# Optimization experiments

Hardware: AMD Instinct MI355X
Metric: run time of the kernel (lower is better)

Reference implementation:

```python
import jax, jax.numpy as jnp
import numpy as np

B, S, D, DM, H, DH, DF, L, T = 4096, 64, 256, 512, 4, 64, 512, 6, 20


def mish(x):
    return x * jnp.tanh(jax.nn.softplus(x))


def layernorm(x, eps=1e-5):
    mu = jnp.mean(x, axis=-1, keepdims=True)
    var = jnp.var(x, axis=-1, keepdims=True)
    return (x - mu) * jax.lax.rsqrt(var + eps)


def setup_inputs() -> dict:
    key = jax.random.key(0)
    ks = iter(jax.random.split(key, 32))
    w = lambda *shape: jax.random.normal(next(ks), shape, dtype=jnp.float32) * 0.02
    inp = {
        'x_t': jax.random.normal(next(ks), (B, S, D), dtype=jnp.float32),
        't': jax.random.randint(next(ks), (B,), 0, T + 1),
        'backbone_latent': jax.random.normal(next(ks), (B, S, DM), dtype=jnp.float32),
        # timestep embedding
        'emb': w(T + 1, D),
        'te_w1': w(D, 4 * D), 'te_b1': jnp.zeros((4 * D,), jnp.float32),
        'te_w2': w(4 * D, D), 'te_b2': jnp.zeros((D,), jnp.float32),
        # cond projection
        'cp_w1': w(DM, D), 'cp_b1': jnp.zeros((D,), jnp.float32),
        'cp_w2': w(D, D), 'cp_b2': jnp.zeros((D,), jnp.float32),
        # stacked per-layer DiT block params [L, ...]
        'adaln_w': w(L, D, 6 * D), 'adaln_b': jnp.zeros((L, 6 * D), jnp.float32),
        'qkv_w': w(L, D, 3 * D), 'qkv_b': jnp.zeros((L, 3 * D), jnp.float32),
        'op_w': w(L, D, D), 'op_b': jnp.zeros((L, D), jnp.float32),
        'ffn_w1': w(L, D, DF), 'ffn_b1': jnp.zeros((L, DF), jnp.float32),
        'ffn_w2': w(L, DF, D), 'ffn_b2': jnp.zeros((L, D), jnp.float32),
        # final adaLN + projection (random here for nontrivial test, zero-init in original)
        'fa_w': w(D, 2 * D), 'fa_b': jnp.zeros((2 * D,), jnp.float32),
        'fp_w': w(D, D), 'fp_b': jnp.zeros((D,), jnp.float32),
    }
    return inp


def _forward(x_t, t, backbone_latent, emb, te_w1, te_b1, te_w2, te_b2,
             cp_w1, cp_b1, cp_w2, cp_b2, adaln_w, adaln_b, qkv_w, qkv_b,
             op_w, op_b, ffn_w1, ffn_b1, ffn_w2, ffn_b2, fa_w, fa_b, fp_w, fp_b):
    # conditioning vector c: [B, D]
    te = emb[t]                                   # [B, D]
    te = mish(te @ te_w1 + te_b1) @ te_w2 + te_b2
    cond = jnp.mean(backbone_latent, axis=1)      # [B, DM]
    cond = mish(cond @ cp_w1 + cp_b1) @ cp_w2 + cp_b2
    c = te + cond
    mc = mish(c)

    x = x_t
    for l in range(L):
        mod = (mc @ adaln_w[l] + adaln_b[l])[:, None, :]   # [B, 1, 6D]
        sh1, sc1, g1, sh2, sc2, g2 = jnp.split(mod, 6, axis=-1)
        # attention sub-block
        h = layernorm(x) * (1.0 + sc1) + sh1
        qkv = (h @ qkv_w[l] + qkv_b[l]).reshape(B, S, 3, H, DH)
        q = qkv[:, :, 0].transpose(0, 2, 1, 3)   # [B, H, S, DH]
        k = qkv[:, :, 1].transpose(0, 2, 1, 3)
        v = qkv[:, :, 2].transpose(0, 2, 1, 3)
        attn = jax.nn.softmax(jnp.einsum('bhsd,bhtd->bhst', q, k) * DH ** -0.5, axis=-1)
        h = jnp.einsum('bhst,bhtd->bhsd', attn, v).transpose(0, 2, 1, 3).reshape(B, S, D)
        h = h @ op_w[l] + op_b[l]
        x = x + g1 * h
        # FFN sub-block
        h = layernorm(x) * (1.0 + sc2) + sh2
        h = mish(h @ ffn_w1[l] + ffn_b1[l]) @ ffn_w2[l] + ffn_b2[l]
        x = x + g2 * h

    mod = (mc @ fa_w + fa_b)[:, None, :]
    shift, scale = jnp.split(mod, 2, axis=-1)
    x = layernorm(x) * (1.0 + scale) + shift
    return x @ fp_w + fp_b


def reference(x_t, t, backbone_latent, emb, te_w1, te_b1, te_w2, te_b2,
              cp_w1, cp_b1, cp_w2, cp_b2, adaln_w, adaln_b, qkv_w, qkv_b,
              op_w, op_b, ffn_w1, ffn_b1, ffn_w2, ffn_b2, fa_w, fa_b, fp_w, fp_b):
    return _forward(x_t, t, backbone_latent, emb, te_w1, te_b1, te_w2, te_b2,
                    cp_w1, cp_b1, cp_w2, cp_b2, adaln_w, adaln_b, qkv_w, qkv_b,
                    op_w, op_b, ffn_w1, ffn_b1, ffn_w2, ffn_b2, fa_w, fa_b, fp_w, fp_b)
```

## Files before the change

### kernel.cpp

```cpp
#include <hip/hip_runtime.h>

typedef unsigned short u16;
typedef float f32x4 __attribute__((ext_vector_type(4)));
typedef __bf16 bf16x8 __attribute__((ext_vector_type(8)));

__device__ __forceinline__ u16 f2b(float f) {
  unsigned u = __builtin_bit_cast(unsigned, f);
  u += 0x7FFF + ((u >> 16) & 1);
  return (u16)(u >> 16);
}

__device__ __forceinline__ float b2f(u16 v) {
  unsigned u = (unsigned)v << 16;
  return __builtin_bit_cast(float, u);
}

__device__ __forceinline__ f32x4 ld_bf4(const u16* p) {
  ushort4 v = *(const ushort4*)p;
  f32x4 r;
  r[0] = b2f(v.x); r[1] = b2f(v.y); r[2] = b2f(v.z); r[3] = b2f(v.w);
  return r;
}

__device__ __forceinline__ float mishf(float x) {
  float e = __expf(fminf(x, 20.f));
  float n = e * (e + 2.f);
  return x * __fdividef(n, n + 2.f);
}

__device__ __forceinline__ void gl_lds16(const void* g, void* l) {
  __builtin_amdgcn_global_load_lds((__attribute__((address_space(1))) void*)g,
                                   (__attribute__((address_space(3))) void*)l, 16, 0, 0);
}

__device__ __forceinline__ bf16x8 ldb8(const u16* p) {
  return __builtin_bit_cast(bf16x8, *(const uint4*)p);
}

__global__ __launch_bounds__(256)
void transpose_w(const float* __restrict__ in, u16* __restrict__ out, int K, int N) {
  __shared__ float tl[64][65];
  const long zoff = (long)blockIdx.z * K * N;
  in += zoff; out += zoff;
  const int n0 = blockIdx.x * 64, k0 = blockIdx.y * 64;
  const int c = threadIdx.x & 63, r0 = threadIdx.x >> 6;
#pragma unroll
  for (int i = 0; i < 16; ++i) {
    int r = i * 4 + r0;
    tl[r][c] = in[(long)(k0 + r) * N + n0 + c];
  }
  __syncthreads();
#pragma unroll
  for (int i = 0; i < 16; ++i) {
    int r = i * 4 + r0;
    out[(long)(n0 + r) * K + k0 + c] = f2b(tl[c][r]);
  }
}

__global__ __launch_bounds__(1024)
void te_table_kernel(const float* __restrict__ emb, const float* __restrict__ w1,
                     const float* __restrict__ b1, const float* __restrict__ w2,
                     const float* __restrict__ b2, float* __restrict__ table) {
  __shared__ float te[256];
  __shared__ float h1[1024];
  __shared__ float red[1024];
  const int tt = blockIdx.x, tid = threadIdx.x;
  if (tid < 256) te[tid] = emb[tt * 256 + tid];
  __syncthreads();
  float a = b1[tid];
#pragma unroll 8
  for (int k = 0; k < 256; ++k) a += te[k] * w1[k * 1024 + tid];
  h1[tid] = mishf(a);
  __syncthreads();
  const int j = tid & 255, kq = tid >> 8;
  float a2 = 0.f;
#pragma unroll 8
  for (int k = kq * 256; k < kq * 256 + 256; ++k) a2 += h1[k] * w2[k * 256 + j];
  red[tid] = a2;
  __syncthreads();
  if (tid < 256)
    table[tt * 256 + tid] = b2[tid] + red[tid] + red[tid + 256] + red[tid + 512] + red[tid + 768];
}

__global__ __launch_bounds__(256)
void cond_mean_kernel(const float* __restrict__ bb, u16* __restrict__ cond) {
  const int b = blockIdx.x, tid = threadIdx.x;
  const float* p = bb + (long)b * 64 * 512;
  for (int d = tid; d < 512; d += 256) {
    float s = 0.f;
#pragma unroll
    for (int t = 0; t < 64; ++t) s += p[t * 512 + d];
    cond[b * 512 + d] = f2b(s * (1.f / 64.f));
  }
}

__global__ __launch_bounds__(256)
void ln_mod(const float* __restrict__ x, const u16* __restrict__ modb,
            int mstride, int shoff, int scoff, u16* __restrict__ out) {
  const int lane = threadIdx.x & 63;
  const long row = (long)blockIdx.x * 4 + (threadIdx.x >> 6);
  const float4 xv = *(const float4*)(x + row * 256 + lane * 4);
  float s1 = xv.x + xv.y + xv.z + xv.w;
  float s2 = xv.x * xv.x + xv.y * xv.y + xv.z * xv.z + xv.w * xv.w;
#pragma unroll
  for (int m = 1; m < 64; m <<= 1) { s1 += __shfl_xor(s1, m); s2 += __shfl_xor(s2, m); }
  const float mean = s1 * (1.f / 256.f);
  float var = s2 * (1.f / 256.f) - mean * mean;
  const float rstd = rsqrtf(fmaxf(var, 0.f) + 1e-5f);
  const long b = row >> 6;
  const f32x4 sc = ld_bf4(modb + b * mstride + scoff + lane * 4);
  const f32x4 sh = ld_bf4(modb + b * mstride + shoff + lane * 4);
  ushort4 o;
  o.x = f2b((xv.x - mean) * rstd * (1.f + sc[0]) + sh[0]);
  o.y = f2b((xv.y - mean) * rstd * (1.f + sc[1]) + sh[1]);
  o.z = f2b((xv.z - mean) * rstd * (1.f + sc[2]) + sh[2]);
  o.w = f2b((xv.w - mean) * rstd * (1.f + sc[3]) + sh[3]);
  *(ushort4*)(out + row * 256 + lane * 4) = o;
}

template <int EPI>
__global__ __launch_bounds__(256)
void gemm_bt(const u16* __restrict__ A, const u16* __restrict__ Bt,
             const float* __restrict__ bias, void* __restrict__ outp,
             const int* __restrict__ tvec, const float* __restrict__ tetab,
             int M, int N, int K) {
  __shared__ __align__(16) u16 As[2][128 * 64];
  __shared__ __align__(16) u16 Bs[2][128 * 64];
  const int tid = threadIdx.x;
  const int lane = tid & 63;
  const int wave = tid >> 6;
  const int wr = (wave >> 1) << 6;
  const int wc = (wave & 1) << 6;
  const long tm = (long)blockIdx.y * 128;
  const long tn = (long)blockIdx.x * 128;
  const u16* Ag = A + tm * K;
  const u16* Bg = Bt + tn * K;
  f32x4 acc[4][4] = {};
  const int kcb = lane >> 4;
  const int swz = lane & 7;
  const int NT = K >> 6;

  auto stage = [&](int t, int buf) {
    const int k0 = t << 6;
#pragma unroll
    for (int i = 0; i < 4; ++i) {
      int c = tid + (i << 8);
      int r = c >> 3;
      int sch = (c & 7) ^ (r & 7);
      gl_lds16(Ag + (long)r * K + k0 + (sch << 3), &As[buf][c << 3]);
    }
#pragma unroll
    for (int i = 0; i < 4; ++i) {
      int c = tid + (i << 8);
      int r = c >> 3;
      int sch = (c & 7) ^ (r & 7);
      gl_lds16(Bg + (long)r * K + k0 + (sch << 3), &Bs[buf][c << 3]);
    }
  };

  stage(0, 0);
  __syncthreads();
  int cur = 0;
  for (int t = 0; t < NT; ++t) {
    if (t + 1 < NT) stage(t + 1, cur ^ 1);
#pragma unroll
    for (int kt = 0; kt < 2; ++kt) {
      const int ko = ((kt * 4 + kcb) ^ swz) << 3;
      bf16x8 av[4], bv[4];
#pragma unroll
      for (int mt = 0; mt < 4; ++mt)
        av[mt] = ldb8(&As[cur][(wr + mt * 16 + (lane & 15)) * 64 + ko]);
#pragma unroll
      for (int nt = 0; nt < 4; ++nt)
        bv[nt] = ldb8(&Bs[cur][(wc + nt * 16 + (lane & 15)) * 64 + ko]);
#pragma unroll
      for (int mt = 0; mt < 4; ++mt)
#pragma unroll
        for (int nt = 0; nt < 4; ++nt)
          acc[mt][nt] = __builtin_amdgcn_mfma_f32_16x16x32_bf16(bv[nt], av[mt], acc[mt][nt], 0, 0, 0);
    }
    __syncthreads();
    cur ^= 1;
  }
  const int rl = lane & 15;
  const int c4 = (lane >> 4) << 2;
  f32x4 b4[4];
#pragma unroll
  for (int nt = 0; nt < 4; ++nt)
    b4[nt] = *(const f32x4*)(bias + (int)tn + wc + nt * 16 + c4);
#pragma unroll
  for (int mt = 0; mt < 4; ++mt) {
    const unsigned row = (unsigned)(tm + wr + mt * 16 + rl);
    const unsigned rb = row * (unsigned)N;
#pragma unroll
    for (int nt = 0; nt < 4; ++nt) {
      const unsigned col = (unsigned)tn + wc + nt * 16 + c4;
      f32x4 v = acc[mt][nt] + b4[nt];
      if constexpr (EPI == 0) {
        ushort4 o;
        o.x = f2b(v[0]); o.y = f2b(v[1]); o.z = f2b(v[2]); o.w = f2b(v[3]);
        *(ushort4*)((u16*)outp + rb + col) = o;
      } else if constexpr (EPI == 1) {
        ushort4 o;
        o.x = f2b(mishf(v[0])); o.y = f2b(mishf(v[1]));
        o.z = f2b(mishf(v[2])); o.w = f2b(mishf(v[3]));
        *(ushort4*)((u16*)outp + rb + col) = o;
      } else if constexpr (EPI == 3) {
        *(f32x4*)((float*)outp + rb + col) = v;
      } else {
        const f32x4 te = *(const f32x4*)(tetab + tvec[row] * 256 + col);
        ushort4 o;
        o.x = f2b(mishf(v[0] + te[0])); o.y = f2b(mishf(v[1] + te[1]));
        o.z = f2b(mishf(v[2] + te[2])); o.w = f2b(mishf(v[3] + te[3]));
        *(ushort4*)((u16*)outp + rb + col) = o;
      }
    }
  }
}

template <int K, bool XF32>
__global__ __launch_bounds__(256)
void gemm_ln(const u16* __restrict__ A, const u16* __restrict__ Bt,
             const float* __restrict__ bias, const void* __restrict__ xin,
             const u16* __restrict__ gptr, int gstride,
             const u16* __restrict__ lnsh, const u16* __restrict__ lnsc, int lnstride,
             u16* __restrict__ xout, u16* __restrict__ hout) {
  __shared__ __align__(16) u16 As[2][64 * 64];
  __shared__ __align__(16) u16 Bs[2][256 * 64];
  const int tid = threadIdx.x, lane = tid & 63, wave = tid >> 6;
  const int wc = wave << 6;
  const long tm = (long)blockIdx.x * 64;
  const u16* Ag = A + tm * K;
  const int rl = lane & 15;
  const int c4 = (lane >> 4) << 2;
  const int swz = lane & 7;
  const int NT = K >> 6;

  auto stage = [&](int t, int buf) {
    const int k0 = t << 6;
#pragma unroll
    for (int i = 0; i < 2; ++i) {
      int c = tid + (i << 8);
      int r = c >> 3;
      int sch = (c & 7) ^ (r & 7);
      gl_lds16(Ag + (long)r * K + k0 + (sch << 3), &As[buf][c << 3]);
    }
#pragma unroll
    for (int i = 0; i < 8; ++i) {
      int c = tid + (i << 8);
      int r = c >> 3;
      int sch = (c & 7) ^ (r & 7);
      gl_lds16(Bt + (long)r * K + k0 + (sch << 3), &Bs[buf][c << 3]);
    }
  };

  stage(0, 0);
  __syncthreads();

  f32x4 acc[4][4] = {};
  int cur = 0;
  for (int t = 0; t < NT; ++t) {
    if (t + 1 < NT) stage(t + 1, cur ^ 1);
#pragma unroll
    for (int kt = 0; kt < 2; ++kt) {
      const int ko = ((kt * 4 + (lane >> 4)) ^ swz) << 3;
      bf16x8 av[4], bv[4];
#pragma unroll
      for (int mt = 0; mt < 4; ++mt)
        av[mt] = ldb8(&As[cur][(mt * 16 + rl) * 64 + ko]);
#pragma unroll
      for (int nt = 0; nt < 4; ++nt)
        bv[nt] = ldb8(&Bs[cur][(wc + nt * 16 + rl) * 64 + ko]);
#pragma unroll
      for (int mt = 0; mt < 4; ++mt)
#pragma unroll
        for (int nt = 0; nt < 4; ++nt)
          acc[mt][nt] = __builtin_amdgcn_mfma_f32_16x16x32_bf16(bv[nt], av[mt], acc[mt][nt], 0, 0, 0);
    }
    __syncthreads();
    cur ^= 1;
  }

  const long b = blockIdx.x;
  float s1[4] = {}, s2[4] = {};
#pragma unroll
  for (int nt = 0; nt < 4; ++nt) {
    const int col = wc + nt * 16 + c4;
    const f32x4 b4 = *(const f32x4*)(bias + col);
    const f32x4 g4 = ld_bf4(gptr + b * gstride + col);
#pragma unroll
    for (int mt = 0; mt < 4; ++mt) {
      const long row = tm + mt * 16 + rl;
      f32x4 x;
      if constexpr (XF32) x = *(const f32x4*)((const float*)xin + row * 256 + col);
      else x = ld_bf4((const u16*)xin + row * 256 + col);
      f32x4 xn = x + g4 * (acc[mt][nt] + b4);
      acc[mt][nt] = xn;
      s1[mt] += xn[0] + xn[1] + xn[2] + xn[3];
      s2[mt] += xn[0] * xn[0] + xn[1] * xn[1] + xn[2] * xn[2] + xn[3] * xn[3];
    }
  }
#pragma unroll
  for (int mt = 0; mt < 4; ++mt) {
    s1[mt] += __shfl_xor(s1[mt], 16); s1[mt] += __shfl_xor(s1[mt], 32);
    s2[mt] += __shfl_xor(s2[mt], 16); s2[mt] += __shfl_xor(s2[mt], 32);
  }
  float* st = (float*)&As[0][0];
  if (lane < 16) {
#pragma unroll
    for (int mt = 0; mt < 4; ++mt) {
      st[wave * 128 + mt * 16 + lane] = s1[mt];
      st[wave * 128 + 64 + mt * 16 + lane] = s2[mt];
    }
  }
  __syncthreads();
  float mean[4], rstd[4];
#pragma unroll
  for (int mt = 0; mt < 4; ++mt) {
    float a = 0.f, q = 0.f;
#pragma unroll
    for (int w2 = 0; w2 < 4; ++w2) {
      a += st[w2 * 128 + mt * 16 + rl];
      q += st[w2 * 128 + 64 + mt * 16 + rl];
    }
    mean[mt] = a * (1.f / 256.f);
    float var = q * (1.f / 256.f) - mean[mt] * mean[mt];
    rstd[mt] = rsqrtf(fmaxf(var, 0.f) + 1e-5f);
  }
#pragma unroll
  for (int nt = 0; nt < 4; ++nt) {
    const int col = wc + nt * 16 + c4;
    const f32x4 sc4 = ld_bf4(lnsc + b * lnstride + col);
    const f32x4 sh4 = ld_bf4(lnsh + b * lnstride + col);
#pragma unroll
    for (int mt = 0; mt < 4; ++mt) {
      const long row = tm + mt * 16 + rl;
      ushort4 xo;
      xo.x = f2b(acc[mt][nt][0]); xo.y = f2b(acc[mt][nt][1]);
      xo.z = f2b(acc[mt][nt][2]); xo.w = f2b(acc[mt][nt][3]);
      *(ushort4*)(xout + row * 256 + col) = xo;
      f32x4 h = (acc[mt][nt] - mean[mt]) * rstd[mt] * (1.f + sc4) + sh4;
      ushort4 o;
      o.x = f2b(h[0]); o.y = f2b(h[1]); o.z = f2b(h[2]); o.w = f2b(h[3]);
      *(ushort4*)(hout + row * 256 + col) = o;
    }
  }
}

__global__ __launch_bounds__(512)
void ffn_fused(const u16* __restrict__ xln, const u16* __restrict__ W1t,
               const float* __restrict__ b1, const u16* __restrict__ W2t,
               const float* __restrict__ b2, const u16* __restrict__ xres,
               const u16* __restrict__ gptr, int gstride,
               const u16* __restrict__ lnsh, const u16* __restrict__ lnsc, int lnstride,
               u16* __restrict__ xout, u16* __restrict__ hout) {
  __shared__ __align__(16) u16 Ax[64 * 256];
  __shared__ __align__(16) u16 Ws[2][256 * 64];
  __shared__ __align__(16) u16 H1[64 * 512];
  const int tid = threadIdx.x, lane = tid & 63, wave = tid >> 6;
  const long b0 = (long)blockIdx.x * 2;
  const int rl = lane & 15;
  const int c4 = (lane >> 4) << 2;
  const int kq = lane >> 4;

  auto stageAx = [&](long b) {
    const u16* src = xln + b * (64 * 256);
#pragma unroll
    for (int i = 0; i < 4; ++i) {
      int c = tid + (i << 9);
      int r = c >> 5, cc = c & 31;
      int sch = (cc & ~7) | ((cc & 7) ^ (r & 7));
      gl_lds16(src + r * 256 + (sch << 3), &Ax[c << 3]);
    }
  };
  auto stageW = [&](const u16* Wsrc, int Kw, int R0, int k0, int buf) {
#pragma unroll
    for (int i = 0; i < 4; ++i) {
      int c = tid + (i << 9);
      int r = c >> 3;
      int sch = (c & 7) ^ (r & 7);
      gl_lds16(Wsrc + (long)(R0 + r) * Kw + k0 + (sch << 3), &Ws[buf][c << 3]);
    }
  };

  stageAx(b0);
  stageW(W1t, 256, 0, 0, 0);
  __syncthreads();
  int cur = 0;

  for (int e = 0; e < 2; ++e) {
    const long b = b0 + e;
    for (int nh = 0; nh < 2; ++nh) {
      f32x4 acc[4][2] = {};
      for (int t = 0; t < 4; ++t) {
        int s = nh * 4 + t;
        if (s < 7) stageW(W1t, 256, ((s + 1) >> 2) * 256, ((s + 1) & 3) * 64, cur ^ 1);
        else stageW(W2t, 512, 0, 0, cur ^ 1);
#pragma unroll
        for (int kt = 0; kt < 2; ++kt) {
          bf16x8 av[4], bv[2];
#pragma unroll
          for (int mt = 0; mt < 4; ++mt) {
            int r = mt * 16 + rl;
            int kc = t * 8 + kt * 4 + kq;
            int slot = (kc & ~7) | ((kc & 7) ^ (r & 7));
            av[mt] = ldb8(&Ax[r * 256 + (slot << 3)]);
          }
#pragma unroll
          for (int nf = 0; nf < 2; ++nf) {
            int wr_ = wave * 32 + nf * 16 + rl;
            int slot = (kt * 4 + kq) ^ (wr_ & 7);
            bv[nf] = ldb8(&Ws[cur][wr_ * 64 + (slot << 3)]);
          }
#pragma unroll
          for (int mt = 0; mt < 4; ++mt)
#pragma unroll
            for (int nf = 0; nf < 2; ++nf)
              acc[mt][nf] = __builtin_amdgcn_mfma_f32_16x16x32_bf16(bv[nf], av[mt], acc[mt][nf], 0, 0, 0);
        }
        __syncthreads();
        cur ^= 1;
      }
#pragma unroll
      for (int nf = 0; nf < 2; ++nf) {
        const int col = nh * 256 + wave * 32 + nf * 16 + c4;
        const f32x4 bb = *(const f32x4*)(b1 + col);
        const int c8 = col >> 3;
        const int sub = (col & 7) << 1;
#pragma unroll
        for (int mt = 0; mt < 4; ++mt) {
          const int r = mt * 16 + rl;
          f32x4 v = acc[mt][nf] + bb;
          ushort4 o;
          o.x = f2b(mishf(v[0])); o.y = f2b(mishf(v[1]));
          o.z = f2b(mishf(v[2])); o.w = f2b(mishf(v[3]));
          int slot = (c8 & ~7) | ((c8 & 7) ^ (r & 7));
          *(ushort4*)((char*)H1 + r * 1024 + (slot << 4) + sub) = o;
        }
      }
    }
    __syncthreads();

    f32x4 acc[4][2] = {};
    for (int t = 0; t < 8; ++t) {
      if (t < 7) stageW(W2t, 512, 0, (t + 1) * 64, cur ^ 1);
      else if (e == 0) stageW(W1t, 256, 0, 0, cur ^ 1);
      if (t == 0 && e == 0) stageAx(b0 + 1);
#pragma unroll
      for (int kt = 0; kt < 2; ++kt) {
        bf16x8 av[4], bv[2];
#pragma unroll
        for (int mt = 0; mt < 4; ++mt) {
          int r = mt * 16 + rl;
          int kc = t * 8 + kt * 4 + kq;
          int slot = (kc & ~7) | ((kc & 7) ^ (r & 7));
          av[mt] = ldb8((const u16*)((const char*)H1 + r * 1024 + (slot << 4)));
        }
#pragma unroll
        for (int nf = 0; nf < 2; ++nf) {
          int wr_ = wave * 32 + nf * 16 + rl;
          int slot = (kt * 4 + kq) ^ (wr_ & 7);
          bv[nf] = ldb8(&Ws[cur][wr_ * 64 + (slot << 3)]);
        }
#pragma unroll
        for (int mt = 0; mt < 4; ++mt)
#pragma unroll
          for (int nf = 0; nf < 2; ++nf)
            acc[mt][nf] = __builtin_amdgcn_mfma_f32_16x16x32_bf16(bv[nf], av[mt], acc[mt][nf], 0, 0, 0);
      }
      __syncthreads();
      cur ^= 1;
    }
    float s1[4] = {}, s2[4] = {};
#pragma unroll
    for (int nf = 0; nf < 2; ++nf) {
      const int col = wave * 32 + nf * 16 + c4;
      const f32x4 bb = *(const f32x4*)(b2 + col);
      const f32x4 g4 = ld_bf4(gptr + b * gstride + col);
#pragma unroll
      for (int mt = 0; mt < 4; ++mt) {
        const long row = b * 64 + mt * 16 + rl;
        f32x4 x = ld_bf4(xres + row * 256 + col);
        f32x4 xn = x + g4 * (acc[mt][nf] + bb);
        acc[mt][nf] = xn;
        s1[mt] += xn[0] + xn[1] + xn[2] + xn[3];
        s2[mt] += xn[0] * xn[0] + xn[1] * xn[1] + xn[2] * xn[2] + xn[3] * xn[3];
      }
    }
#pragma unroll
    for (int mt = 0; mt < 4; ++mt) {
      s1[mt] += __shfl_xor(s1[mt], 16); s1[mt] += __shfl_xor(s1[mt], 32);
      s2[mt] += __shfl_xor(s2[mt], 16); s2[mt] += __shfl_xor(s2[mt], 32);
    }
    float* st = (float*)&H1[0];
    if (lane < 16) {
#pragma unroll
      for (int mt = 0; mt < 4; ++mt) {
        st[wave * 128 + mt * 16 + lane] = s1[mt];
        st[wave * 128 + 64 + mt * 16 + lane] = s2[mt];
      }
    }
    __syncthreads();
    float mean[4], rstd[4];
#pragma unroll
    for (int mt = 0; mt < 4; ++mt) {
      float a = 0.f, q = 0.f;
#pragma unroll
      for (int w2 = 0; w2 < 8; ++w2) {
        a += st[w2 * 128 + mt * 16 + rl];
        q += st[w2 * 128 + 64 + mt * 16 + rl];
      }
      mean[mt] = a * (1.f / 256.f);
      float var = q * (1.f / 256.f) - mean[mt] * mean[mt];
      rstd[mt] = rsqrtf(fmaxf(var, 0.f) + 1e-5f);
    }
#pragma unroll
    for (int nf = 0; nf < 2; ++nf) {
      const int col = wave * 32 + nf * 16 + c4;
      const f32x4 sc4 = ld_bf4(lnsc + b * lnstride + col);
      const f32x4 sh4 = ld_bf4(lnsh + b * lnstride + col);
#pragma unroll
      for (int mt = 0; mt < 4; ++mt) {
        const long row = b * 64 + mt * 16 + rl;
        ushort4 xo;
        xo.x = f2b(acc[mt][nf][0]); xo.y = f2b(acc[mt][nf][1]);
        xo.z = f2b(acc[mt][nf][2]); xo.w = f2b(acc[mt][nf][3]);
        *(ushort4*)(xout + row * 256 + col) = xo;
        f32x4 h = (acc[mt][nf] - mean[mt]) * rstd[mt] * (1.f + sc4) + sh4;
        ushort4 o;
        o.x = f2b(h[0]); o.y = f2b(h[1]); o.z = f2b(h[2]); o.w = f2b(h[3]);
        *(ushort4*)(hout + row * 256 + col) = o;
      }
    }
    __syncthreads();
  }
}

__global__ __launch_bounds__(128)
void attn_kernel(const u16* __restrict__ qkv, u16* __restrict__ out) {
  __shared__ __align__(16) u16 vt_s[2][64 * 72];
  __shared__ __align__(16) u16 p_s[2][64 * 72];
  const int lane = threadIdx.x & 63;
  const int wave = threadIdx.x >> 6;
  const long b = blockIdx.x >> 1;
  const int h = ((blockIdx.x & 1) << 1) | wave;
  u16* vt = vt_s[wave];
  u16* pl = p_s[wave];
  const u16* base = qkv + b * (64 * 768);
#pragma unroll
  for (int it = 0; it < 8; ++it) {
    int chunk = it * 64 + lane;
    int t = chunk >> 3, dhb = (chunk & 7) << 3;
    union { uint4 u; u16 s[8]; } uv;
    uv.u = *(const uint4*)(base + t * 768 + 512 + h * 64 + dhb);
#pragma unroll
    for (int j = 0; j < 8; ++j) vt[(dhb + j) * 72 + t] = uv.s[j];
  }
  const u16* qb = base + h * 64;
  const u16* kb = base + 256 + h * 64;
  f32x4 sacc[4][4] = {};
#pragma unroll
  for (int kt = 0; kt < 2; ++kt) {
    bf16x8 qa[4], kv[4];
#pragma unroll
    for (int mt = 0; mt < 4; ++mt)
      qa[mt] = ldb8(qb + ((lane & 15) + mt * 16) * 768 + kt * 32 + ((lane >> 4) << 3));
#pragma unroll
    for (int nt = 0; nt < 4; ++nt)
      kv[nt] = ldb8(kb + ((lane & 15) + nt * 16) * 768 + kt * 32 + ((lane >> 4) << 3));
#pragma unroll
    for (int mt = 0; mt < 4; ++mt)
#pragma unroll
      for (int nt = 0; nt < 4; ++nt)
        sacc[mt][nt] = __builtin_amdgcn_mfma_f32_16x16x32_bf16(qa[mt], kv[nt], sacc[mt][nt], 0, 0, 0);
  }
  const float scale = 0.125f;
#pragma unroll
  for (int mt = 0; mt < 4; ++mt) {
#pragma unroll
    for (int r = 0; r < 4; ++r) {
      float mx = fmaxf(fmaxf(sacc[mt][0][r], sacc[mt][1][r]), fmaxf(sacc[mt][2][r], sacc[mt][3][r]));
#pragma unroll
      for (int m = 1; m <= 8; m <<= 1) mx = fmaxf(mx, __shfl_xor(mx, m));
      float p[4];
      float sum = 0.f;
#pragma unroll
      for (int nt = 0; nt < 4; ++nt) { p[nt] = __expf((sacc[mt][nt][r] - mx) * scale); sum += p[nt]; }
#pragma unroll
      for (int m = 1; m <= 8; m <<= 1) sum += __shfl_xor(sum, m);
      const float rinv = 1.f / sum;
      const int s = mt * 16 + ((lane >> 4) << 2) + r;
#pragma unroll
      for (int nt = 0; nt < 4; ++nt) pl[s * 72 + nt * 16 + (lane & 15)] = f2b(p[nt] * rinv);
    }
  }
  __syncthreads();
  f32x4 oacc[4][4] = {};
#pragma unroll
  for (int kt = 0; kt < 2; ++kt) {
    bf16x8 pa[4], vv[4];
#pragma unroll
    for (int mt = 0; mt < 4; ++mt)
      pa[mt] = ldb8(pl + ((lane & 15) + mt * 16) * 72 + kt * 32 + ((lane >> 4) << 3));
#pragma unroll
    for (int nt = 0; nt < 4; ++nt)
      vv[nt] = ldb8(vt + ((lane & 15) + nt * 16) * 72 + kt * 32 + ((lane >> 4) << 3));
#pragma unroll
    for (int mt = 0; mt < 4; ++mt)
#pragma unroll
      for (int nt = 0; nt < 4; ++nt)
        oacc[mt][nt] = __builtin_amdgcn_mfma_f32_16x16x32_bf16(vv[nt], pa[mt], oacc[mt][nt], 0, 0, 0);
  }
  u16* ob = out + b * (64 * 256) + h * 64;
#pragma unroll
  for (int mt = 0; mt < 4; ++mt)
#pragma unroll
    for (int nt = 0; nt < 4; ++nt) {
      const int s = mt * 16 + (lane & 15);
      const int d4 = nt * 16 + ((lane >> 4) << 2);
      ushort4 o;
      o.x = f2b(oacc[mt][nt][0]); o.y = f2b(oacc[mt][nt][1]);
      o.z = f2b(oacc[mt][nt][2]); o.w = f2b(oacc[mt][nt][3]);
      *(ushort4*)(ob + s * 256 + d4) = o;
    }
}

extern "C" void kernel_launch(void* const* d_in, const int* in_sizes, int n_in,
                              void* d_out, int out_size, void* d_ws, size_t ws_size,
                              hipStream_t stream) {
  (void)in_sizes; (void)n_in; (void)out_size; (void)ws_size;
  const int B = 4096, L = 6;
  const long BSr = (long)B * 64;

  const float* x_t = (const float*)d_in[0];
  const int* tvec = (const int*)d_in[1];
  const float* backbone = (const float*)d_in[2];
  const float* emb = (const float*)d_in[3];
  const float* te_w1 = (const float*)d_in[4];
  const float* te_b1 = (const float*)d_in[5];
  const float* te_w2 = (const float*)d_in[6];
  const float* te_b2 = (const float*)d_in[7];
  const float* cp_w1 = (const float*)d_in[8];
  const float* cp_b1 = (const float*)d_in[9];
  const float* cp_w2 = (const float*)d_in[10];
  const float* cp_b2 = (const float*)d_in[11];
  const float* adaln_w = (const float*)d_in[12];
  const float* adaln_b = (const float*)d_in[13];
  const float* qkv_w = (const float*)d_in[14];
  const float* qkv_b = (const float*)d_in[15];
  const float* op_w = (const float*)d_in[16];
  const float* op_b = (const float*)d_in[17];
  const float* ffn_w1 = (const float*)d_in[18];
  const float* ffn_b1 = (const float*)d_in[19];
  const float* ffn_w2 = (const float*)d_in[20];
  const float* ffn_b2 = (const float*)d_in[21];
  const float* fa_w = (const float*)d_in[22];
  const float* fa_b = (const float*)d_in[23];
  const float* fp_w = (const float*)d_in[24];
  const float* fp_b = (const float*)d_in[25];

  char* w = (char*)d_ws;
  auto alloc = [&](size_t bytes) { char* p = w; w += (bytes + 255) & ~(size_t)255; return p; };
  u16* WT_cp1 = (u16*)alloc(256L * 512 * 2);
  u16* WT_cp2 = (u16*)alloc(256L * 256 * 2);
  u16* WT_adaln = (u16*)alloc(6L * 1536 * 256 * 2);
  u16* WT_qkv = (u16*)alloc(6L * 768 * 256 * 2);
  u16* WT_op = (u16*)alloc(6L * 256 * 256 * 2);
  u16* WT_f1 = (u16*)alloc(6L * 512 * 256 * 2);
  u16* WT_f2 = (u16*)alloc(6L * 256 * 512 * 2);
  u16* WT_fa = (u16*)alloc(512L * 256 * 2);
  u16* WT_fp = (u16*)alloc(256L * 256 * 2);
  float* te_tab = (float*)alloc(21L * 256 * 4);
  u16* cond = (u16*)alloc(4096L * 512 * 2);
  u16* c1 = (u16*)alloc(4096L * 256 * 2);
  u16* mc = (u16*)alloc(4096L * 256 * 2);
  u16* modb6 = (u16*)alloc(4096L * 9216 * 2);
  u16* famod = (u16*)alloc(4096L * 512 * 2);
  u16* hbuf = (u16*)alloc(BSr * 256 * 2);
  u16* qkvbuf = (u16*)alloc(BSr * 768 * 2);
  u16* xbuf = (u16*)d_out;

  transpose_w<<<dim3(4, 8, 1), 256, 0, stream>>>(cp_w1, WT_cp1, 512, 256);
  transpose_w<<<dim3(4, 4, 1), 256, 0, stream>>>(cp_w2, WT_cp2, 256, 256);
  transpose_w<<<dim3(24, 4, 6), 256, 0, stream>>>(adaln_w, WT_adaln, 256, 1536);
  transpose_w<<<dim3(12, 4, 6), 256, 0, stream>>>(qkv_w, WT_qkv, 256, 768);
  transpose_w<<<dim3(4, 4, 6), 256, 0, stream>>>(op_w, WT_op, 256, 256);
  transpose_w<<<dim3(8, 4, 6), 256, 0, stream>>>(ffn_w1, WT_f1, 256, 512);
  transpose_w<<<dim3(4, 8, 6), 256, 0, stream>>>(ffn_w2, WT_f2, 512, 256);
  transpose_w<<<dim3(8, 4, 1), 256, 0, stream>>>(fa_w, WT_fa, 256, 512);
  transpose_w<<<dim3(4, 4, 1), 256, 0, stream>>>(fp_w, WT_fp, 256, 256);

  te_table_kernel<<<21, 1024, 0, stream>>>(emb, te_w1, te_b1, te_w2, te_b2, te_tab);
  cond_mean_kernel<<<4096, 256, 0, stream>>>(backbone, cond);

  gemm_bt<1><<<dim3(2, 32), 256, 0, stream>>>(cond, WT_cp1, cp_b1, c1, nullptr, nullptr, 4096, 256, 512);
  gemm_bt<4><<<dim3(2, 32), 256, 0, stream>>>(c1, WT_cp2, cp_b2, mc, tvec, te_tab, 4096, 256, 256);
  gemm_bt<0><<<dim3(4, 32), 256, 0, stream>>>(mc, WT_fa, fa_b, famod, nullptr, nullptr, 4096, 512, 256);
  gemm_bt<0><<<dim3(72, 32), 256, 0, stream>>>(mc, WT_adaln, adaln_b, modb6, nullptr, nullptr, 4096, 9216, 256);

  ln_mod<<<BSr / 4, 256, 0, stream>>>(x_t, modb6, 9216, 0, 256, hbuf);

  for (int l = 0; l < L; ++l) {
    const u16* mb = modb6 + (long)l * 1536;
    gemm_bt<0><<<dim3(6, BSr / 128), 256, 0, stream>>>(hbuf, WT_qkv + (long)l * 768 * 256, qkv_b + l * 768,
                                                       qkvbuf, nullptr, nullptr, (int)BSr, 768, 256);
    attn_kernel<<<B * 2, 128, 0, stream>>>(qkvbuf, hbuf);
    if (l == 0)
      gemm_ln<256, true><<<BSr / 64, 256, 0, stream>>>(hbuf, WT_op, op_b, x_t, mb + 512, 9216,
                                                       mb + 768, mb + 1024, 9216, xbuf, hbuf);
    else
      gemm_ln<256, false><<<BSr / 64, 256, 0, stream>>>(hbuf, WT_op + (long)l * 256 * 256, op_b + l * 256,
                                                        xbuf, mb + 512, 9216, mb + 768, mb + 1024, 9216, xbuf, hbuf);
    const u16* nsh = (l < 5) ? (mb + 1536) : famod;
    const u16* nsc = (l < 5) ? (mb + 1536 + 256) : (famod + 256);
    const int nstride = (l < 5) ? 9216 : 512;
    ffn_fused<<<BSr / 128, 512, 0, stream>>>(hbuf, WT_f1 + (long)l * 512 * 256, ffn_b1 + l * 512,
                                             WT_f2 + (long)l * 256 * 512, ffn_b2 + l * 256,
                                             xbuf, mb + 1280, 9216, nsh, nsc, nstride, xbuf, hbuf);
  }
  gemm_bt<3><<<dim3(2, BSr / 128), 256, 0, stream>>>(hbuf, WT_fp, fp_b, d_out, nullptr, nullptr, (int)BSr, 256, 256);
}
```

Baseline: 6.250 ms.

## Merge final adaLN GEMM into adaLN GEMM; process two batches per gemm_ln block

```diff
diff --git a/kernel.cpp b/kernel.cpp
--- a/kernel.cpp
+++ b/kernel.cpp
@@ -55,6 +55,14 @@
     int r = i * 4 + r0;
     out[(long)(n0 + r) * K + k0 + c] = f2b(tl[c][r]);
   }
+}
+
+__global__ __launch_bounds__(256)
+void concat_bias(const float* __restrict__ a, const float* __restrict__ b,
+                 float* __restrict__ out) {
+  int i = blockIdx.x * 256 + threadIdx.x;
+  if (i < 9216) out[i] = a[i];
+  else if (i < 9728) out[i] = b[i - 9216];
 }
 
 __global__ __launch_bounds__(1024)
@@ -229,14 +237,14 @@
   __shared__ __align__(16) u16 Bs[2][256 * 64];
   const int tid = threadIdx.x, lane = tid & 63, wave = tid >> 6;
   const int wc = wave << 6;
-  const long tm = (long)blockIdx.x * 64;
-  const u16* Ag = A + tm * K;
+  const long b0 = (long)blockIdx.x * 2;
   const int rl = lane & 15;
   const int c4 = (lane >> 4) << 2;
   const int swz = lane & 7;
   const int NT = K >> 6;
 
-  auto stage = [&](int t, int buf) {
+  auto stageA = [&](long b, int t, int buf) {
+    const u16* Ag = A + b * 64 * K;
     const int k0 = t << 6;
 #pragma unroll
     for (int i = 0; i < 2; ++i) {
@@ -245,6 +253,9 @@
       int sch = (c & 7) ^ (r & 7);
       gl_lds16(Ag + (long)r * K + k0 + (sch << 3), &As[buf][c << 3]);
     }
+  };
+  auto stageB = [&](int t, int buf) {
+    const int k0 = t << 6;
 #pragma unroll
     for (int i = 0; i < 8; ++i) {
       int c = tid + (i << 8);
@@ -254,96 +265,102 @@
     }
   };
 
-  stage(0, 0);
+  stageA(b0, 0, 0);
+  stageB(0, 0);
   __syncthreads();
-
-  f32x4 acc[4][4] = {};
   int cur = 0;
-  for (int t = 0; t < NT; ++t) {
-    if (t + 1 < NT) stage(t + 1, cur ^ 1);
-#pragma unroll
-    for (int kt = 0; kt < 2; ++kt) {
-      const int ko = ((kt * 4 + (lane >> 4)) ^ swz) << 3;
-      bf16x8 av[4], bv[4];
-#pragma unroll
-      for (int mt = 0; mt < 4; ++mt)
-        av[mt] = ldb8(&As[cur][(mt * 16 + rl) * 64 + ko]);
-#pragma unroll
-      for (int nt = 0; nt < 4; ++nt)
-        bv[nt] = ldb8(&Bs[cur][(wc + nt * 16 + rl) * 64 + ko]);
-#pragma unroll
-      for (int mt = 0; mt < 4; ++mt)
+
+  for (int e = 0; e < 2; ++e) {
+    const long b = b0 + e;
+    const long tm = b * 64;
+    f32x4 acc[4][4] = {};
+    for (int t = 0; t < NT; ++t) {
+      if (t + 1 < NT) { stageA(b, t + 1, cur ^ 1); stageB(t + 1, cur ^ 1); }
+      else if (e == 0) { stageA(b0 + 1, 0, cur ^ 1); stageB(0, cur ^ 1); }
+#pragma unroll
+      for (int kt = 0; kt < 2; ++kt) {
+        const int ko = ((kt * 4 + (lane >> 4)) ^ swz) << 3;
+        bf16x8 av[4], bv[4];
+#pragma unroll
+        for (int mt = 0; mt < 4; ++mt)
+          av[mt] = ldb8(&As[cur][(mt * 16 + rl) * 64 + ko]);
 #pragma unroll
         for (int nt = 0; nt < 4; ++nt)
-          acc[mt][nt] = __builtin_amdgcn_mfma_f32_16x16x32_bf16(bv[nt], av[mt], acc[mt][nt], 0, 0, 0);
+          bv[nt] = ldb8(&Bs[cur][(wc + nt * 16 + rl) * 64 + ko]);
+#pragma unroll
+        for (int mt = 0; mt < 4; ++mt)
+#pragma unroll
+          for (int nt = 0; nt < 4; ++nt)
+            acc[mt][nt] = __builtin_amdgcn_mfma_f32_16x16x32_bf16(bv[nt], av[mt], acc[mt][nt], 0, 0, 0);
+      }
+      __syncthreads();
+      cur ^= 1;
+    }
+
+    float s1[4] = {}, s2[4] = {};
+#pragma unroll
+    for (int nt = 0; nt < 4; ++nt) {
+      const int col = wc + nt * 16 + c4;
+      const f32x4 b4 = *(const f32x4*)(bias + col);
+      const f32x4 g4 = ld_bf4(gptr + b * gstride + col);
+#pragma unroll
+      for (int mt = 0; mt < 4; ++mt) {
+        const long row = tm + mt * 16 + rl;
+        f32x4 x;
+        if constexpr (XF32) x = *(const f32x4*)((const float*)xin + row * 256 + col);
+        else x = ld_bf4((const u16*)xin + row * 256 + col);
+        f32x4 xn = x + g4 * (acc[mt][nt] + b4);
+        acc[mt][nt] = xn;
+        s1[mt] += xn[0] + xn[1] + xn[2] + xn[3];
+        s2[mt] += xn[0] * xn[0] + xn[1] * xn[1] + xn[2] * xn[2] + xn[3] * xn[3];
+      }
+    }
+#pragma unroll
+    for (int mt = 0; mt < 4; ++mt) {
+      s1[mt] += __shfl_xor(s1[mt], 16); s1[mt] += __shfl_xor(s1[mt], 32);
+      s2[mt] += __shfl_xor(s2[mt], 16); s2[mt] += __shfl_xor(s2[mt], 32);
+    }
+    float* st = (float*)&As[cur ^ 1][0];
+    if (lane < 16) {
+#pragma unroll
+      for (int mt = 0; mt < 4; ++mt) {
+        st[wave * 128 + mt * 16 + lane] = s1[mt];
+        st[wave * 128 + 64 + mt * 16 + lane] = s2[mt];
+      }
     }
     __syncthreads();
-    cur ^= 1;
-  }
-
-  const long b = blockIdx.x;
-  float s1[4] = {}, s2[4] = {};
-#pragma unroll
-  for (int nt = 0; nt < 4; ++nt) {
-    const int col = wc + nt * 16 + c4;
-    const f32x4 b4 = *(const f32x4*)(bias + col);
-    const f32x4 g4 = ld_bf4(gptr + b * gstride + col);
+    float mean[4], rstd[4];
 #pragma unroll
     for (int mt = 0; mt < 4; ++mt) {
-      const long row = tm + mt * 16 + rl;
-      f32x4 x;
-      if constexpr (XF32) x = *(const f32x4*)((const float*)xin + row * 256 + col);
-      else x = ld_bf4((const u16*)xin + row * 256 + col);
-      f32x4 xn = x + g4 * (acc[mt][nt] + b4);
-      acc[mt][nt] = xn;
-      s1[mt] += xn[0] + xn[1] + xn[2] + xn[3];
-      s2[mt] += xn[0] * xn[0] + xn[1] * xn[1] + xn[2] * xn[2] + xn[3] * xn[3];
-    }
-  }
-#pragma unroll
-  for (int mt = 0; mt < 4; ++mt) {
-    s1[mt] += __shfl_xor(s1[mt], 16); s1[mt] += __shfl_xor(s1[mt], 32);
-    s2[mt] += __shfl_xor(s2[mt], 16); s2[mt] += __shfl_xor(s2[mt], 32);
-  }
-  float* st = (float*)&As[0][0];
-  if (lane < 16) {
-#pragma unroll
-    for (int mt = 0; mt < 4; ++mt) {
-      st[wave * 128 + mt * 16 + lane] = s1[mt];
-      st[wave * 128 + 64 + mt * 16 + lane] = s2[mt];
-    }
-  }
-  __syncthreads();
-  float mean[4], rstd[4];
-#pragma unroll
-  for (int mt = 0; mt < 4; ++mt) {
-    float a = 0.f, q = 0.f;
-#pragma unroll
-    for (int w2 = 0; w2 < 4; ++w2) {
-      a += st[w2 * 128 + mt * 16 + rl];
-      q += st[w2 * 128 + 64 + mt * 16 + rl];
-    }
-    mean[mt] = a * (1.f / 256.f);
-    float var = q * (1.f / 256.f) - mean[mt] * mean[mt];
-    rstd[mt] = rsqrtf(fmaxf(var, 0.f) + 1e-5f);
-  }
-#pragma unroll
-  for (int nt = 0; nt < 4; ++nt) {
-    const int col = wc + nt * 16 + c4;
-    const f32x4 sc4 = ld_bf4(lnsc + b * lnstride + col);
-    const f32x4 sh4 = ld_bf4(lnsh + b * lnstride + col);
-#pragma unroll
-    for (int mt = 0; mt < 4; ++mt) {
-      const long row = tm + mt * 16 + rl;
-      ushort4 xo;
-      xo.x = f2b(acc[mt][nt][0]); xo.y = f2b(acc[mt][nt][1]);
-      xo.z = f2b(acc[mt][nt][2]); xo.w = f2b(acc[mt][nt][3]);
-      *(ushort4*)(xout + row * 256 + col) = xo;
-      f32x4 h = (acc[mt][nt] - mean[mt]) * rstd[mt] * (1.f + sc4) + sh4;
-      ushort4 o;
-      o.x = f2b(h[0]); o.y = f2b(h[1]); o.z = f2b(h[2]); o.w = f2b(h[3]);
-      *(ushort4*)(hout + row * 256 + col) = o;
-    }
+      float a = 0.f, q = 0.f;
+#pragma unroll
+      for (int w2 = 0; w2 < 4; ++w2) {
+        a += st[w2 * 128 + mt * 16 + rl];
+        q += st[w2 * 128 + 64 + mt * 16 + rl];
+      }
+      mean[mt] = a * (1.f / 256.f);
+      float var = q * (1.f / 256.f) - mean[mt] * mean[mt];
+      rstd[mt] = rsqrtf(fmaxf(var, 0.f) + 1e-5f);
+    }
+#pragma unroll
+    for (int nt = 0; nt < 4; ++nt) {
+      const int col = wc + nt * 16 + c4;
+      const f32x4 sc4 = ld_bf4(lnsc + b * lnstride + col);
+      const f32x4 sh4 = ld_bf4(lnsh + b * lnstride + col);
+#pragma unroll
+      for (int mt = 0; mt < 4; ++mt) {
+        const long row = tm + mt * 16 + rl;
+        ushort4 xo;
+        xo.x = f2b(acc[mt][nt][0]); xo.y = f2b(acc[mt][nt][1]);
+        xo.z = f2b(acc[mt][nt][2]); xo.w = f2b(acc[mt][nt][3]);
+        *(ushort4*)(xout + row * 256 + col) = xo;
+        f32x4 h = (acc[mt][nt] - mean[mt]) * rstd[mt] * (1.f + sc4) + sh4;
+        ushort4 o;
+        o.x = f2b(h[0]); o.y = f2b(h[1]); o.z = f2b(h[2]); o.w = f2b(h[3]);
+        *(ushort4*)(hout + row * 256 + col) = o;
+      }
+    }
+    __syncthreads();
   }
 }
 
@@ -663,42 +680,41 @@
   auto alloc = [&](size_t bytes) { char* p = w; w += (bytes + 255) & ~(size_t)255; return p; };
   u16* WT_cp1 = (u16*)alloc(256L * 512 * 2);
   u16* WT_cp2 = (u16*)alloc(256L * 256 * 2);
-  u16* WT_adaln = (u16*)alloc(6L * 1536 * 256 * 2);
+  u16* WT_all = (u16*)alloc(9728L * 256 * 2);
   u16* WT_qkv = (u16*)alloc(6L * 768 * 256 * 2);
   u16* WT_op = (u16*)alloc(6L * 256 * 256 * 2);
   u16* WT_f1 = (u16*)alloc(6L * 512 * 256 * 2);
   u16* WT_f2 = (u16*)alloc(6L * 256 * 512 * 2);
-  u16* WT_fa = (u16*)alloc(512L * 256 * 2);
   u16* WT_fp = (u16*)alloc(256L * 256 * 2);
+  float* bias_all = (float*)alloc(9728L * 4);
   float* te_tab = (float*)alloc(21L * 256 * 4);
   u16* cond = (u16*)alloc(4096L * 512 * 2);
   u16* c1 = (u16*)alloc(4096L * 256 * 2);
   u16* mc = (u16*)alloc(4096L * 256 * 2);
-  u16* modb6 = (u16*)alloc(4096L * 9216 * 2);
-  u16* famod = (u16*)alloc(4096L * 512 * 2);
+  u16* modb6 = (u16*)alloc(4096L * 9728 * 2);
   u16* hbuf = (u16*)alloc(BSr * 256 * 2);
   u16* qkvbuf = (u16*)alloc(BSr * 768 * 2);
   u16* xbuf = (u16*)d_out;
 
   transpose_w<<<dim3(4, 8, 1), 256, 0, stream>>>(cp_w1, WT_cp1, 512, 256);
   transpose_w<<<dim3(4, 4, 1), 256, 0, stream>>>(cp_w2, WT_cp2, 256, 256);
-  transpose_w<<<dim3(24, 4, 6), 256, 0, stream>>>(adaln_w, WT_adaln, 256, 1536);
+  transpose_w<<<dim3(24, 4, 6), 256, 0, stream>>>(adaln_w, WT_all, 256, 1536);
+  transpose_w<<<dim3(8, 4, 1), 256, 0, stream>>>(fa_w, WT_all + 9216L * 256, 256, 512);
   transpose_w<<<dim3(12, 4, 6), 256, 0, stream>>>(qkv_w, WT_qkv, 256, 768);
   transpose_w<<<dim3(4, 4, 6), 256, 0, stream>>>(op_w, WT_op, 256, 256);
   transpose_w<<<dim3(8, 4, 6), 256, 0, stream>>>(ffn_w1, WT_f1, 256, 512);
   transpose_w<<<dim3(4, 8, 6), 256, 0, stream>>>(ffn_w2, WT_f2, 512, 256);
-  transpose_w<<<dim3(8, 4, 1), 256, 0, stream>>>(fa_w, WT_fa, 256, 512);
   transpose_w<<<dim3(4, 4, 1), 256, 0, stream>>>(fp_w, WT_fp, 256, 256);
+  concat_bias<<<38, 256, 0, stream>>>(adaln_b, fa_b, bias_all);
 
   te_table_kernel<<<21, 1024, 0, stream>>>(emb, te_w1, te_b1, te_w2, te_b2, te_tab);
   cond_mean_kernel<<<4096, 256, 0, stream>>>(backbone, cond);
 
   gemm_bt<1><<<dim3(2, 32), 256, 0, stream>>>(cond, WT_cp1, cp_b1, c1, nullptr, nullptr, 4096, 256, 512);
   gemm_bt<4><<<dim3(2, 32), 256, 0, stream>>>(c1, WT_cp2, cp_b2, mc, tvec, te_tab, 4096, 256, 256);
-  gemm_bt<0><<<dim3(4, 32), 256, 0, stream>>>(mc, WT_fa, fa_b, famod, nullptr, nullptr, 4096, 512, 256);
-  gemm_bt<0><<<dim3(72, 32), 256, 0, stream>>>(mc, WT_adaln, adaln_b, modb6, nullptr, nullptr, 4096, 9216, 256);
-
-  ln_mod<<<BSr / 4, 256, 0, stream>>>(x_t, modb6, 9216, 0, 256, hbuf);
+  gemm_bt<0><<<dim3(76, 32), 256, 0, stream>>>(mc, WT_all, bias_all, modb6, nullptr, nullptr, 4096, 9728, 256);
+
+  ln_mod<<<BSr / 4, 256, 0, stream>>>(x_t, modb6, 9728, 0, 256, hbuf);
 
   for (int l = 0; l < L; ++l) {
     const u16* mb = modb6 + (long)l * 1536;
@@ -706,17 +722,16 @@
                                                        qkvbuf, nullptr, nullptr, (int)BSr, 768, 256);
     attn_kernel<<<B * 2, 128, 0, stream>>>(qkvbuf, hbuf);
     if (l == 0)
-      gemm_ln<256, true><<<BSr / 64, 256, 0, stream>>>(hbuf, WT_op, op_b, x_t, mb + 512, 9216,
-                                                       mb + 768, mb + 1024, 9216, xbuf, hbuf);
+      gemm_ln<256, true><<<BSr / 128, 256, 0, stream>>>(hbuf, WT_op, op_b, x_t, mb + 512, 9728,
+                                                        mb + 768, mb + 1024, 9728, xbuf, hbuf);
     else
-      gemm_ln<256, false><<<BSr / 64, 256, 0, stream>>>(hbuf, WT_op + (long)l * 256 * 256, op_b + l * 256,
-                                                        xbuf, mb + 512, 9216, mb + 768, mb + 1024, 9216, xbuf, hbuf);
-    const u16* nsh = (l < 5) ? (mb + 1536) : famod;
-    const u16* nsc = (l < 5) ? (mb + 1536 + 256) : (famod + 256);
-    const int nstride = (l < 5) ? 9216 : 512;
+      gemm_ln<256, false><<<BSr / 128, 256, 0, stream>>>(hbuf, WT_op + (long)l * 256 * 256, op_b + l * 256,
+                                                         xbuf, mb + 512, 9728, mb + 768, mb + 1024, 9728, xbuf, hbuf);
+    const u16* nsh = (l < 5) ? (mb + 1536) : (modb6 + 9216);
+    const u16* nsc = (l < 5) ? (mb + 1536 + 256) : (modb6 + 9216 + 256);
     ffn_fused<<<BSr / 128, 512, 0, stream>>>(hbuf, WT_f1 + (long)l * 512 * 256, ffn_b1 + l * 512,
                                              WT_f2 + (long)l * 256 * 512, ffn_b2 + l * 256,
-                                             xbuf, mb + 1280, 9216, nsh, nsc, nstride, xbuf, hbuf);
+                                             xbuf, mb + 1280, 9728, nsh, nsc, 9728, xbuf, hbuf);
   }
   gemm_bt<3><<<dim3(2, BSr / 128), 256, 0, stream>>>(hbuf, WT_fp, fp_b, d_out, nullptr, nullptr, (int)BSr, 256, 256);
 }
```

Result: slower. 6.526 ms (+4.4%).
